# Kernel optimization log

Measured on AMD Instinct MI355X. Metric: run time of the kernel, lower is better.

## Reference

```python
import jax, jax.numpy as jnp
import numpy as np
import math

H_DIM = 1024
N_HEADS = 16
B, T = 2, 2048


def setup_inputs() -> dict:
    key = jax.random.key(0)
    ks = jax.random.split(key, 9)
    scale = 1.0 / math.sqrt(H_DIM)
    x = jax.random.normal(ks[0], (B, T, H_DIM), dtype=jnp.float32)
    Wq = jax.random.normal(ks[1], (H_DIM, H_DIM), dtype=jnp.float32) * scale
    Wk = jax.random.normal(ks[2], (H_DIM, H_DIM), dtype=jnp.float32) * scale
    Wv = jax.random.normal(ks[3], (H_DIM, H_DIM), dtype=jnp.float32) * scale
    Wp = jax.random.normal(ks[4], (H_DIM, H_DIM), dtype=jnp.float32) * scale
    bq = jnp.zeros((H_DIM,), dtype=jnp.float32)
    bk = jnp.zeros((H_DIM,), dtype=jnp.float32)
    bv = jnp.zeros((H_DIM,), dtype=jnp.float32)
    bp = jnp.zeros((H_DIM,), dtype=jnp.float32)
    return {"x": x, "Wq": Wq, "bq": bq, "Wk": Wk, "bk": bk,
            "Wv": Wv, "bv": bv, "Wp": Wp, "bp": bp}


def _attention(x, Wq, bq, Wk, bk, Wv, bv, Wp, bp):
    Bx, Tx, C = x.shape
    N = N_HEADS
    D = C // N
    # torch Linear: x @ W.T + b
    q = (x @ Wq.T + bq).reshape(Bx, Tx, N, D).transpose(0, 2, 1, 3)  # [B,N,T,D]
    k = (x @ Wk.T + bk).reshape(Bx, Tx, N, D).transpose(0, 2, 1, 3)
    v = (x @ Wv.T + bv).reshape(Bx, Tx, N, D).transpose(0, 2, 1, 3)
    scores = jnp.einsum('bntd,bnsd->bnts', q, k) / math.sqrt(D)  # [B,N,T,T]
    causal = jnp.tril(jnp.ones((Tx, Tx), dtype=bool))
    scores = jnp.where(causal[None, None], scores, -jnp.inf)
    probs = jax.nn.softmax(scores, axis=-1)
    attn = jnp.einsum('bnts,bnsd->bntd', probs, v)  # [B,N,T,D]
    attn = attn.transpose(0, 2, 1, 3).reshape(Bx, Tx, C)
    return attn @ Wp.T + bp


def reference(x, Wq, bq, Wk, bk, Wv, bv, Wp, bp):
    return _attention(x, Wq, bq, Wk, bk, Wv, bv, Wp, bp)
```

## Files before the change

### kernel.cpp

```cpp
#include <hip/hip_runtime.h>
#include <hip/hip_bf16.h>
#include <math.h>

#define TSEQ 2048
#define CDIM 1024
#define NHEADS 16
#define DHEAD 64
#define BSZ 2
#define MROWS (BSZ * TSEQ)

typedef __attribute__((ext_vector_type(8))) short short8;
typedef __attribute__((ext_vector_type(4))) short short4v;
typedef __attribute__((ext_vector_type(4))) float f32x4;

__device__ inline f32x4 mfma16(short8 a, short8 b, f32x4 c) {
    return __builtin_amdgcn_mfma_f32_16x16x32_bf16(a, b, c, 0, 0, 0);
}

__device__ inline short f2bf(float f) {
    __hip_bfloat16 h = __float2bfloat16(f);
    return __builtin_bit_cast(short, h);
}
__device__ inline float bf2f(short s) {
    __hip_bfloat16 h = __builtin_bit_cast(__hip_bfloat16, s);
    return __bfloat162float(h);
}

__global__ __launch_bounds__(256) void convx_kernel(const float* __restrict__ x,
                                                    short* __restrict__ xb) {
    size_t off = (size_t)(blockIdx.x * 256 + threadIdx.x) * 8;
    float4 a = *(const float4*)(x + off);
    float4 b = *(const float4*)(x + off + 4);
    short8 h;
    h[0] = f2bf(a.x); h[1] = f2bf(a.y); h[2] = f2bf(a.z); h[3] = f2bf(a.w);
    h[4] = f2bf(b.x); h[5] = f2bf(b.y); h[6] = f2bf(b.z); h[7] = f2bf(b.w);
    *(short8*)(xb + off) = h;
}

__global__ __launch_bounds__(256, 3) void gemm_qkv(
    const short* __restrict__ xb, const float* __restrict__ Wq,
    const float* __restrict__ Wk, const float* __restrict__ Wv,
    const float* __restrict__ bq, const float* __restrict__ bk,
    const float* __restrict__ bv, short* __restrict__ qws,
    short* __restrict__ kws, short* __restrict__ vtws) {
    __shared__ __attribute__((aligned(16))) short a_lds[128][72];
    __shared__ __attribute__((aligned(16))) short b_lds[128][72];

    const int tid = threadIdx.x;
    const int lane = tid & 63;
    const int wv = tid >> 6;
    const int wr = wv >> 1, wc = wv & 1;
    const int l15 = lane & 15, l4 = lane >> 4;
    const int mbase = blockIdx.x * 128;
    const int which = blockIdx.y >> 3;
    const int nbase = (blockIdx.y & 7) * 128;
    const float* Wf = which == 0 ? Wq : (which == 1 ? Wk : Wv);
    const float* bias = which == 0 ? bq : (which == 1 ? bk : bv);

    f32x4 acc[4][4];
#pragma unroll
    for (int i = 0; i < 4; ++i)
#pragma unroll
        for (int j = 0; j < 4; ++j) acc[i][j] = f32x4{0.f, 0.f, 0.f, 0.f};

    const int ar = tid >> 3;
    const int ag = (tid & 7) * 8;
    const int br = tid >> 4;
    const int bg = (tid & 15) * 4;
    const short* aptr = xb + (size_t)(mbase + ar) * CDIM + ag;
    const float* bptr = Wf + (size_t)(nbase + br) * CDIM + bg;

    short8 apre[4];
    float4 bpre[8];
#pragma unroll
    for (int it = 0; it < 4; ++it)
        apre[it] = *(const short8*)(aptr + (size_t)(32 * it) * CDIM);
#pragma unroll
    for (int it = 0; it < 8; ++it)
        bpre[it] = *(const float4*)(bptr + (size_t)(16 * it) * CDIM);

    for (int k0 = 0; k0 < CDIM; k0 += 64) {
        __syncthreads();
#pragma unroll
        for (int it = 0; it < 4; ++it)
            *(short8*)&a_lds[ar + 32 * it][ag] = apre[it];
#pragma unroll
        for (int it = 0; it < 8; ++it) {
            short4v h;
            h.x = f2bf(bpre[it].x); h.y = f2bf(bpre[it].y);
            h.z = f2bf(bpre[it].z); h.w = f2bf(bpre[it].w);
            *(short4v*)&b_lds[br + 16 * it][bg] = h;
        }
        __syncthreads();
        if (k0 + 64 < CDIM) {
#pragma unroll
            for (int it = 0; it < 4; ++it)
                apre[it] = *(const short8*)(aptr + (size_t)(32 * it) * CDIM + k0 + 64);
#pragma unroll
            for (int it = 0; it < 8; ++it)
                bpre[it] = *(const float4*)(bptr + (size_t)(16 * it) * CDIM + k0 + 64);
        }

#pragma unroll
        for (int kk = 0; kk < 2; ++kk) {
            short8 af[4], bfr[4];
#pragma unroll
            for (int i = 0; i < 4; ++i)
                af[i] = *(const short8*)&a_lds[wr * 64 + i * 16 + l15][kk * 32 + l4 * 8];
#pragma unroll
            for (int j = 0; j < 4; ++j)
                bfr[j] = *(const short8*)&b_lds[wc * 64 + j * 16 + l15][kk * 32 + l4 * 8];
#pragma unroll
            for (int i = 0; i < 4; ++i)
#pragma unroll
                for (int j = 0; j < 4; ++j)
                    acc[i][j] = mfma16(af[i], bfr[j], acc[i][j]);
        }
    }

    if (which < 2) {
        short* dst = which == 0 ? qws : kws;
#pragma unroll
        for (int i = 0; i < 4; ++i) {
            int mrow = mbase + wr * 64 + i * 16 + l4 * 4;
#pragma unroll
            for (int j = 0; j < 4; ++j) {
                int o = nbase + wc * 64 + j * 16 + l15;
                int n = o >> 6, d = o & 63;
                float bval = bias[o];
#pragma unroll
                for (int r = 0; r < 4; ++r) {
                    int mm = mrow + r;
                    int bb = mm >> 11;
                    int t = mm & (TSEQ - 1);
                    dst[(((size_t)bb * NHEADS + n) * TSEQ + t) * DHEAD + d] =
                        f2bf(acc[i][j][r] + bval);
                }
            }
        }
    } else {
#pragma unroll
        for (int i = 0; i < 4; ++i) {
            int mrow = mbase + wr * 64 + i * 16 + l4 * 4;
            int bb = mrow >> 11;
            int t = mrow & (TSEQ - 1);
#pragma unroll
            for (int j = 0; j < 4; ++j) {
                int o = nbase + wc * 64 + j * 16 + l15;
                int n = o >> 6, d = o & 63;
                float bval = bias[o];
                short4v h4;
#pragma unroll
                for (int r = 0; r < 4; ++r) h4[r] = f2bf(acc[i][j][r] + bval);
                *(short4v*)&vtws[(((size_t)bb * NHEADS + n) * DHEAD + d) * TSEQ + t] = h4;
            }
        }
    }
}

__global__ __launch_bounds__(256) void gemm_p(
    const short* __restrict__ attn, const float* __restrict__ Wp,
    const float* __restrict__ bp, float* __restrict__ out) {
    __shared__ __attribute__((aligned(16))) short a_lds[64][40];
    __shared__ __attribute__((aligned(16))) short b_lds[128][40];

    const int tid = threadIdx.x;
    const int lane = tid & 63;
    const int wv = tid >> 6;
    const int wr = wv >> 1, wc = wv & 1;
    const int l15 = lane & 15, l4 = lane >> 4;
    const int mbase = blockIdx.x * 64;
    const int nbase = blockIdx.y * 128;

    f32x4 acc[2][4];
#pragma unroll
    for (int i = 0; i < 2; ++i)
#pragma unroll
        for (int j = 0; j < 4; ++j) acc[i][j] = f32x4{0.f, 0.f, 0.f, 0.f};

    const int arow = tid >> 2;
    const int acol = (tid & 3) * 8;
    const int brow = tid >> 3;
    const int bcol = (tid & 7) * 4;
    const short* aptr = attn + (size_t)(mbase + arow) * CDIM + acol;
    const float* bptr = Wp + (size_t)(nbase + brow) * CDIM + bcol;

    short8 apre;
    float4 bpre[4];
    apre = *(const short8*)(aptr);
#pragma unroll
    for (int it = 0; it < 4; ++it)
        bpre[it] = *(const float4*)(bptr + (size_t)(it * 32) * CDIM);

    for (int k0 = 0; k0 < CDIM; k0 += 32) {
        __syncthreads();
        *(short8*)&a_lds[arow][acol] = apre;
#pragma unroll
        for (int it = 0; it < 4; ++it) {
            short4v h;
            h.x = f2bf(bpre[it].x); h.y = f2bf(bpre[it].y);
            h.z = f2bf(bpre[it].z); h.w = f2bf(bpre[it].w);
            *(short4v*)&b_lds[brow + it * 32][bcol] = h;
        }
        __syncthreads();
        if (k0 + 32 < CDIM) {
            apre = *(const short8*)(aptr + k0 + 32);
#pragma unroll
            for (int it = 0; it < 4; ++it)
                bpre[it] = *(const float4*)(bptr + (size_t)(it * 32) * CDIM + k0 + 32);
        }

        short8 af[2], bfr[4];
#pragma unroll
        for (int i = 0; i < 2; ++i)
            af[i] = *(const short8*)&a_lds[wr * 32 + i * 16 + l15][l4 * 8];
#pragma unroll
        for (int j = 0; j < 4; ++j)
            bfr[j] = *(const short8*)&b_lds[wc * 64 + j * 16 + l15][l4 * 8];
#pragma unroll
        for (int i = 0; i < 2; ++i)
#pragma unroll
            for (int j = 0; j < 4; ++j)
                acc[i][j] = mfma16(af[i], bfr[j], acc[i][j]);
    }

#pragma unroll
    for (int i = 0; i < 2; ++i) {
        int mrow = mbase + wr * 32 + i * 16 + l4 * 4;
#pragma unroll
        for (int j = 0; j < 4; ++j) {
            int o = nbase + wc * 64 + j * 16 + l15;
            float bval = bp[o];
#pragma unroll
            for (int r = 0; r < 4; ++r)
                out[(size_t)(mrow + r) * CDIM + o] = acc[i][j][r] + bval;
        }
    }
}

__global__ __launch_bounds__(256) void attn_kernel(
    const short* __restrict__ q, const short* __restrict__ k,
    const short* __restrict__ vt, short* __restrict__ attn_out) {
    __shared__ __attribute__((aligned(16))) short k_lds[64][64];
    __shared__ __attribute__((aligned(16))) short vt_lds[64][64];
    __shared__ __attribute__((aligned(16))) short p_lds[4][16][80];

    const int tid = threadIdx.x;
    const int w = tid >> 6;
    const int lane = tid & 63;
    const int l15 = lane & 15;
    const int l4 = lane >> 4;
    const int h = blockIdx.x;
    const int qtile = gridDim.y - 1 - blockIdx.y;
    const int qb = qtile * 64;
    const int wrow0 = qb + w * 16;

    short8 qf[2];
#pragma unroll
    for (int kh = 0; kh < 2; ++kh) {
        const short* qp = q + ((size_t)h * TSEQ + wrow0 + l15) * DHEAD + kh * 32 + l4 * 8;
        short8 t8 = *(const short8*)qp;
#pragma unroll
        for (int e = 0; e < 8; ++e) t8[e] = f2bf(bf2f(t8[e]) * 0.125f);
        qf[kh] = t8;
    }

    float l_run[4];
    f32x4 o_acc[4];
#pragma unroll
    for (int r = 0; r < 4; ++r) l_run[r] = 0.f;
#pragma unroll
    for (int dt = 0; dt < 4; ++dt) o_acc[dt] = f32x4{0.f, 0.f, 0.f, 0.f};

    const int ntiles = qtile + 1;
    const int srow = tid >> 3;
    const int sgrp = tid & 7;

    short8 kpre[2], vpre[2];
#pragma unroll
    for (int it = 0; it < 2; ++it) {
        int row = srow + it * 32;
        kpre[it] = *(const short8*)(k + ((size_t)h * TSEQ + row) * DHEAD + sgrp * 8);
        vpre[it] = *(const short8*)(vt + ((size_t)h * DHEAD + row) * TSEQ + sgrp * 8);
    }

    for (int kvt = 0; kvt < ntiles; ++kvt) {
        const int kvbase = kvt * 64;
        __syncthreads();
#pragma unroll
        for (int it = 0; it < 2; ++it) {
            int row = srow + it * 32;
            int gs = sgrp ^ (row & 7);
            *(short8*)&k_lds[row][gs * 8] = kpre[it];
            *(short8*)&vt_lds[row][gs * 8] = vpre[it];
        }
        __syncthreads();
        if (kvt + 1 < ntiles) {
            int kvb2 = kvbase + 64;
#pragma unroll
            for (int it = 0; it < 2; ++it) {
                int row = srow + it * 32;
                kpre[it] = *(const short8*)(k + ((size_t)h * TSEQ + kvb2 + row) * DHEAD + sgrp * 8);
                vpre[it] = *(const short8*)(vt + ((size_t)h * DHEAD + row) * TSEQ + kvb2 + sgrp * 8);
            }
        }

        f32x4 s[4];
#pragma unroll
        for (int jt = 0; jt < 4; ++jt) {
            int row = jt * 16 + l15;
            int sw = row & 7;
            short8 kf0 = *(const short8*)&k_lds[row][(l4 ^ sw) * 8];
            short8 kf1 = *(const short8*)&k_lds[row][((4 + l4) ^ sw) * 8];
            f32x4 a = f32x4{0.f, 0.f, 0.f, 0.f};
            a = mfma16(qf[0], kf0, a);
            a = mfma16(qf[1], kf1, a);
            s[jt] = a;
        }

        const bool needmask = (kvbase + 63 > wrow0);
#pragma unroll
        for (int r = 0; r < 4; ++r) {
            int qrow = wrow0 + l4 * 4 + r;
            float lp = 0.f;
#pragma unroll
            for (int jt = 0; jt < 4; ++jt) {
                float x = s[jt][r];
                if (needmask && (kvbase + jt * 16 + l15 > qrow)) x = -INFINITY;
                float e = __expf(fminf(x, 60.f));
                lp += e;
                p_lds[w][l4 * 4 + r][jt * 16 + l15] = f2bf(e);
            }
            l_run[r] += lp;
        }

        short8 pa0 = *(const short8*)&p_lds[w][l15][l4 * 8];
        short8 pa1 = *(const short8*)&p_lds[w][l15][32 + l4 * 8];
#pragma unroll
        for (int dt = 0; dt < 4; ++dt) {
            int row = dt * 16 + l15;
            int sw = row & 7;
            short8 vf0 = *(const short8*)&vt_lds[row][(l4 ^ sw) * 8];
            short8 vf1 = *(const short8*)&vt_lds[row][((4 + l4) ^ sw) * 8];
            o_acc[dt] = mfma16(pa0, vf0, o_acc[dt]);
            o_acc[dt] = mfma16(pa1, vf1, o_acc[dt]);
        }
    }

#pragma unroll
    for (int r = 0; r < 4; ++r) {
        float l = l_run[r];
#pragma unroll
        for (int mk = 1; mk < 16; mk <<= 1) l += __shfl_xor(l, mk);
        l_run[r] = 1.0f / l;
    }
    const int b = h >> 4, n = h & 15;
#pragma unroll
    for (int dt = 0; dt < 4; ++dt) {
#pragma unroll
        for (int r = 0; r < 4; ++r) {
            int t = wrow0 + l4 * 4 + r;
            attn_out[((size_t)b * TSEQ + t) * CDIM + n * DHEAD + dt * 16 + l15] =
                f2bf(o_acc[dt][r] * l_run[r]);
        }
    }
}

extern "C" void kernel_launch(void* const* d_in, const int* in_sizes, int n_in,
                              void* d_out, int out_size, void* d_ws, size_t ws_size,
                              hipStream_t stream) {
    const float* x  = (const float*)d_in[0];
    const float* Wq = (const float*)d_in[1];
    const float* bq = (const float*)d_in[2];
    const float* Wk = (const float*)d_in[3];
    const float* bk = (const float*)d_in[4];
    const float* Wv = (const float*)d_in[5];
    const float* bv = (const float*)d_in[6];
    const float* Wp = (const float*)d_in[7];
    const float* bp = (const float*)d_in[8];

    char* ws = (char*)d_ws;
    const size_t SZ = (size_t)MROWS * CDIM * sizeof(short);
    short* qws  = (short*)(ws);
    short* kws  = (short*)(ws + SZ);
    short* vtws = (short*)(ws + 2 * SZ);
    short* xb   = (short*)(ws + 3 * SZ);
    short* attn = xb;

    convx_kernel<<<2048, 256, 0, stream>>>(x, xb);
    gemm_qkv<<<dim3(MROWS / 128, 24), 256, 0, stream>>>(xb, Wq, Wk, Wv, bq, bk, bv,
                                                         qws, kws, vtws);
    attn_kernel<<<dim3(BSZ * NHEADS, TSEQ / 64), 256, 0, stream>>>(qws, kws, vtws, attn);
    gemm_p<<<dim3(MROWS / 64, CDIM / 128), 256, 0, stream>>>(attn, Wp, bp, (float*)d_out);
}
```

Measured before the change: 113.9 us.

## Fold softmax scale into Q projection, use exp2, truncate bf16, swizzle block order

The Q projection epilogue now multiplies by 0.125*log2(e), so the attention kernel no longer rescales Q on load and can call exp2 directly. The fminf clamp is gone, and probabilities are truncated to bf16 by bit masking, with the row sum built from the same truncated values. Both GEMMs remap block indices so neighbouring workgroups share operand tiles, which is meant to improve L2 reuse. Dropping the clamp means no max subtraction guards against overflow, and truncation adds a small rounding bias.

```diff
diff --git a/kernel.cpp b/kernel.cpp
--- a/kernel.cpp
+++ b/kernel.cpp
@@ -8,6 +8,7 @@
 #define DHEAD 64
 #define BSZ 2
 #define MROWS (BSZ * TSEQ)
+#define SCALE_Q 0.18033688f
 
 typedef __attribute__((ext_vector_type(8))) short short8;
 typedef __attribute__((ext_vector_type(4))) short short4v;
@@ -20,10 +21,6 @@
 __device__ inline short f2bf(float f) {
     __hip_bfloat16 h = __float2bfloat16(f);
     return __builtin_bit_cast(short, h);
-}
-__device__ inline float bf2f(short s) {
-    __hip_bfloat16 h = __builtin_bit_cast(__hip_bfloat16, s);
-    return __bfloat162float(h);
 }
 
 __global__ __launch_bounds__(256) void convx_kernel(const float* __restrict__ x,
@@ -51,9 +48,13 @@
     const int wv = tid >> 6;
     const int wr = wv >> 1, wc = wv & 1;
     const int l15 = lane & 15, l4 = lane >> 4;
-    const int mbase = blockIdx.x * 128;
-    const int which = blockIdx.y >> 3;
-    const int nbase = (blockIdx.y & 7) * 128;
+
+    const int hw = blockIdx.x + 32 * blockIdx.y;
+    const int work = (hw & 7) * 96 + (hw >> 3);
+    const int mbase = (work & 31) * 128;
+    const int wy = work >> 5;
+    const int which = wy >> 3;
+    const int nbase = (wy & 7) * 128;
     const float* Wf = which == 0 ? Wq : (which == 1 ? Wk : Wv);
     const float* bias = which == 0 ? bq : (which == 1 ? bk : bv);
 
@@ -120,6 +121,7 @@
 
     if (which < 2) {
         short* dst = which == 0 ? qws : kws;
+        const float scale = which == 0 ? SCALE_Q : 1.0f;
 #pragma unroll
         for (int i = 0; i < 4; ++i) {
             int mrow = mbase + wr * 64 + i * 16 + l4 * 4;
@@ -134,7 +136,7 @@
                     int bb = mm >> 11;
                     int t = mm & (TSEQ - 1);
                     dst[(((size_t)bb * NHEADS + n) * TSEQ + t) * DHEAD + d] =
-                        f2bf(acc[i][j][r] + bval);
+                        f2bf((acc[i][j][r] + bval) * scale);
                 }
             }
         }
@@ -169,8 +171,11 @@
     const int wv = tid >> 6;
     const int wr = wv >> 1, wc = wv & 1;
     const int l15 = lane & 15, l4 = lane >> 4;
-    const int mbase = blockIdx.x * 64;
-    const int nbase = blockIdx.y * 128;
+
+    const int hw = blockIdx.x + 64 * blockIdx.y;
+    const int work = (hw & 7) * 64 + (hw >> 3);
+    const int mbase = (work & 63) * 64;
+    const int nbase = (work >> 6) * 128;
 
     f32x4 acc[2][4];
 #pragma unroll
@@ -257,13 +262,9 @@
 
     short8 qf[2];
 #pragma unroll
-    for (int kh = 0; kh < 2; ++kh) {
-        const short* qp = q + ((size_t)h * TSEQ + wrow0 + l15) * DHEAD + kh * 32 + l4 * 8;
-        short8 t8 = *(const short8*)qp;
-#pragma unroll
-        for (int e = 0; e < 8; ++e) t8[e] = f2bf(bf2f(t8[e]) * 0.125f);
-        qf[kh] = t8;
-    }
+    for (int kh = 0; kh < 2; ++kh)
+        qf[kh] = *(const short8*)(q + ((size_t)h * TSEQ + wrow0 + l15) * DHEAD +
+                                  kh * 32 + l4 * 8);
 
     float l_run[4];
     f32x4 o_acc[4];
@@ -327,9 +328,10 @@
             for (int jt = 0; jt < 4; ++jt) {
                 float x = s[jt][r];
                 if (needmask && (kvbase + jt * 16 + l15 > qrow)) x = -INFINITY;
-                float e = __expf(fminf(x, 60.f));
-                lp += e;
-                p_lds[w][l4 * 4 + r][jt * 16 + l15] = f2bf(e);
+                float e = __builtin_exp2f(x);
+                unsigned int eb = __builtin_bit_cast(unsigned int, e);
+                p_lds[w][l4 * 4 + r][jt * 16 + l15] = (short)(eb >> 16);
+                lp += __builtin_bit_cast(float, eb & 0xffff0000u);
             }
             l_run[r] += lp;
         }
```

Result: slower. 125.9 us (+10.5%).
